# Kernel optimization log

Hardware: AMD Instinct MI355X
Metric: run time of the kernel (lower is better)

## Reference

```python
import jax, jax.numpy as jnp
import numpy as np

B, S, E, H = 2, 2048, 2048, 16
D = E // H  # head_dim = 128


def _rope_tables(seq_len, dim):
    # standard RoPE: theta_i = 10000^(-2i/dim), angles duplicated over pair halves
    inv_freq = 1.0 / (10000.0 ** (np.arange(0, dim, 2, dtype=np.float32) / dim))
    angles = np.arange(seq_len, dtype=np.float32)[:, None] * inv_freq[None, :]  # [S, D/2]
    angles = np.concatenate([angles, angles], axis=-1)  # [S, D]
    return jnp.asarray(np.cos(angles)), jnp.asarray(np.sin(angles))


def setup_inputs() -> dict:
    key = jax.random.key(0)
    ks = jax.random.split(key, 10)
    sc = 1.0 / np.sqrt(E)
    cos, sin = _rope_tables(S, D)
    mask = jnp.tril(jnp.ones((S, S), dtype=bool))[None, None]  # causal [1,1,S,S]
    return {
        "x_q": jax.random.normal(ks[0], (B, S, E), jnp.float32),
        "x_kv": jax.random.normal(ks[1], (B, S, E), jnp.float32),
        "cos": cos,
        "sin": sin,
        "wq": jax.random.normal(ks[2], (E, E), jnp.float32) * sc,
        "bq": jax.random.normal(ks[3], (E,), jnp.float32) * 0.01,
        "wk": jax.random.normal(ks[4], (E, E), jnp.float32) * sc,
        "bk": jax.random.normal(ks[5], (E,), jnp.float32) * 0.01,
        "wv": jax.random.normal(ks[6], (E, E), jnp.float32) * sc,
        "bv": jax.random.normal(ks[7], (E,), jnp.float32) * 0.01,
        "wo": jax.random.normal(ks[8], (E, E), jnp.float32) * sc,
        "bo": jax.random.normal(ks[9], (E,), jnp.float32) * 0.01,
        "mask": mask,
    }


def _apply_rope(x, cos, sin):
    # x: [B,H,S,D]; cos/sin: [S,D]. rotate-half convention.
    x1, x2 = jnp.split(x, 2, axis=-1)
    rot = jnp.concatenate([-x2, x1], axis=-1)
    return x * cos[None, None] + rot * sin[None, None]


def reference(x_q, x_kv, cos, sin, wq, bq, wk, bk, wv, bv, wo, bo, mask):
    b, sq, _ = x_q.shape
    skv = x_kv.shape[1]
    q = (x_q @ wq.T + bq).reshape(b, sq, H, D).transpose(0, 2, 1, 3)   # [B,H,Sq,D]
    k = (x_kv @ wk.T + bk).reshape(b, skv, H, D).transpose(0, 2, 1, 3)
    v = (x_kv @ wv.T + bv).reshape(b, skv, H, D).transpose(0, 2, 1, 3)
    q = _apply_rope(q, cos, sin)
    k = _apply_rope(k, cos, sin)
    scores = jnp.einsum("bhqd,bhkd->bhqk", q, k) / jnp.sqrt(jnp.float32(D))
    scores = jnp.where(mask, scores, jnp.float32(-1e9))
    w = jax.nn.softmax(scores, axis=-1)  # dropout p=0 -> identity
    out = jnp.einsum("bhqk,bhkd->bhqd", w, v)
    out = out.transpose(0, 2, 1, 3).reshape(b, sq, H * D)
    return out @ wo.T + bo
```

## Files before the change

kernel.cpp:

```cpp
#include <hip/hip_runtime.h>
#include <hip/hip_bf16.h>

#define Bb 2
#define Ss 2048
#define Ee 2048
#define Hh 16
#define Dd 128
#define Mrows (Bb*Ss)

typedef short short8 __attribute__((ext_vector_type(8)));
typedef float f32x4 __attribute__((ext_vector_type(4)));

__device__ __forceinline__ unsigned short bf_rne(float f) {
    unsigned u = __builtin_bit_cast(unsigned, f);
    u += 0x7fffu + ((u >> 16) & 1u);
    return (unsigned short)(u >> 16);
}
__device__ __forceinline__ float bf2f(unsigned short x) {
    unsigned u = ((unsigned)x) << 16;
    return __builtin_bit_cast(float, u);
}
__device__ __forceinline__ void load_lds16(const void* g, void* l) {
    __builtin_amdgcn_global_load_lds(
        (const __attribute__((address_space(1))) unsigned int*)g,
        (__attribute__((address_space(3))) unsigned int*)l, 16, 0, 0);
}

__global__ void cast_all_kernel(const float4* __restrict__ xq, const float4* __restrict__ xkv,
                                const float4* __restrict__ wq, const float4* __restrict__ wk,
                                const float4* __restrict__ wv, const float4* __restrict__ wo,
                                ushort4* __restrict__ out) {
    int i = blockIdx.x * 256 + threadIdx.x;
    const float4* src;
    int rel;
    if (i < 2097152)       { src = xq;  rel = i; }
    else if (i < 4194304)  { src = xkv; rel = i - 2097152; }
    else if (i < 5242880)  { src = wq;  rel = i - 4194304; }
    else if (i < 6291456)  { src = wk;  rel = i - 5242880; }
    else if (i < 7340032)  { src = wv;  rel = i - 6291456; }
    else                   { src = wo;  rel = i - 7340032; }
    float4 v = src[rel];
    ushort4 o;
    o.x = bf_rne(v.x); o.y = bf_rne(v.y); o.z = bf_rne(v.z); o.w = bf_rne(v.w);
    out[i] = o;
}

#define NTK 64
#define BUFB 24576

__device__ __forceinline__ void gemm_core(
    const short* __restrict__ A, const short* __restrict__ W,
    int m0, int n0, char* lds, f32x4 (&acc)[8][4], int tid)
{
    const int wid  = tid >> 6, lane = tid & 63;
    const int wr   = wid >> 1, wc   = wid & 1;
    const int quad = lane >> 4, l16 = lane & 15;
    const int lr   = lane >> 3, sl  = lane & 7;
    const int g    = sl ^ lr;
    const int grow = 2*(wid*8 + lr) + (g >> 2);
    const int kcol = (g & 3) * 8;
    const int cx16 = ((((l16 & 1) << 2) + quad) ^ ((l16 >> 1) & 7)) << 4;
    const int arow = (l16 >> 1) << 7;

    const short* Ab = A + (size_t)(m0 + grow) * Ee + kcol;
    const short* Wb = W + (size_t)(n0 + grow) * Ee + kcol;

    auto stageTile = [&](int kt, int so) {
        const short* a = Ab + kt * 32;
        const short* w = Wb + kt * 32;
        #pragma unroll
        for (int i = 0; i < 4; ++i)
            load_lds16(a + (size_t)i*64*Ee, lds + so + i*4096 + wid*1024);
        #pragma unroll
        for (int i = 0; i < 2; ++i)
            load_lds16(w + (size_t)i*64*Ee, lds + so + 16384 + i*4096 + wid*1024);
    };

    stageTile(0, 0);
    stageTile(1, BUFB);
    asm volatile("s_waitcnt vmcnt(6)\n\ts_barrier" ::: "memory");

    int bo = 0, so = 2*BUFB;
    for (int t = 0; t < NTK; ++t) {
        if (t + 2 < NTK) stageTile(t + 2, so);

        const char* Abase = lds + bo + wr*8192 + arow + cx16;
        const char* Bbase = lds + bo + 16384 + wc*4096 + arow + cx16;
        short8 af[8], bf[4];
        #pragma unroll
        for (int i = 0; i < 8; ++i) af[i] = *(const short8*)(Abase + i*1024);
        #pragma unroll
        for (int j = 0; j < 4; ++j) bf[j] = *(const short8*)(Bbase + j*1024);

        __builtin_amdgcn_s_setprio(1);
        #pragma unroll
        for (int i = 0; i < 8; ++i)
            #pragma unroll
            for (int j = 0; j < 4; ++j)
                acc[i][j] = __builtin_amdgcn_mfma_f32_16x16x32_bf16(af[i], bf[j], acc[i][j], 0, 0, 0);
        __builtin_amdgcn_s_setprio(0);

        if (t == NTK - 1) break;
        if (t < NTK - 2) asm volatile("s_waitcnt vmcnt(6)\n\ts_barrier" ::: "memory");
        else             asm volatile("s_waitcnt vmcnt(0)\n\ts_barrier" ::: "memory");
        bo = (bo == 2*BUFB) ? 0 : bo + BUFB;
        so = (so == 2*BUFB) ? 0 : so + BUFB;
    }
}

__global__ __launch_bounds__(256, 2) void qkv_gemm(
    const short* __restrict__ xq, const short* __restrict__ xkv,
    const short* __restrict__ wq, const short* __restrict__ wk, const short* __restrict__ wv,
    const float* __restrict__ bq, const float* __restrict__ bk, const float* __restrict__ bv,
    short* __restrict__ Qr, short* __restrict__ Kr, short* __restrict__ VT)
{
    __shared__ __align__(16) char lds[73728];
    const int tid  = threadIdx.x;
    const int wid  = tid >> 6, lane = tid & 63;
    const int quad = lane >> 4, l16 = lane & 15;
    const int wr   = wid >> 1, wc   = wid & 1;
    const int m0   = blockIdx.x * 256;
    const int sub  = blockIdx.y >> 4;
    const int nb   = blockIdx.y & 15;
    const int n0   = nb * 128;

    const short* A = (sub == 0) ? xq : xkv;
    const short* W = (sub == 0) ? wq : (sub == 1) ? wk : wv;
    const float* bias = (sub == 0) ? bq : (sub == 1) ? bk : bv;

    f32x4 acc[8][4] = {};
    gemm_core(A, W, m0, n0, lds, acc, tid);

    const int b0 = m0 >> 11;
    const int s0 = m0 & (Ss - 1);

    if (sub < 2) {
        short* out = sub ? Kr : Qr;
        #pragma unroll
        for (int i = 0; i < 8; ++i)
            #pragma unroll
            for (int j = 0; j < 4; ++j)
                #pragma unroll
                for (int r = 0; r < 4; ++r) {
                    int gm = m0 + wr*128 + i*16 + quad*4 + r;
                    int d  = wc*64 + j*16 + l16;
                    float v = acc[i][j][r] + bias[n0 + d];
                    int b = gm >> 11, s = gm & (Ss - 1);
                    out[(((size_t)(b*Hh + nb)) * Ss + s) * Dd + d] = (short)bf_rne(v);
                }
    } else {
        __syncthreads();
        short* T = (short*)lds + wid * 8704;
        #pragma unroll
        for (int i = 0; i < 8; ++i)
            #pragma unroll
            for (int j = 0; j < 4; ++j)
                #pragma unroll
                for (int r = 0; r < 4; ++r) {
                    int dl  = j*16 + l16;
                    int slc = i*16 + quad*4 + r;
                    T[dl*136 + slc] = (short)bf_rne(acc[i][j][r] + bias[n0 + wc*64 + dl]);
                }
        __syncthreads();
        #pragma unroll
        for (int ss = 0; ss < 16; ++ss) {
            short8 v = *(const short8*)&T[lane*136 + ss*8];
            int dg = wc*64 + lane;
            int sg = s0 + wr*128 + ss*8;
            *(short8*)&VT[(((size_t)(b0*Hh + nb)) * Dd + dg) * Ss + sg] = v;
        }
    }
}

__global__ __launch_bounds__(256, 2) void oproj_gemm(
    const short* __restrict__ A, const short* __restrict__ W,
    const float* __restrict__ bias, float* __restrict__ Cf)
{
    __shared__ __align__(16) char lds[73728];
    const int tid  = threadIdx.x;
    const int wid  = tid >> 6, lane = tid & 63;
    const int quad = lane >> 4, l16 = lane & 15;
    const int wr   = wid >> 1, wc   = wid & 1;
    const int m0   = blockIdx.x * 256;
    const int n0   = blockIdx.y * 128;

    f32x4 acc[8][4] = {};
    gemm_core(A, W, m0, n0, lds, acc, tid);

    #pragma unroll
    for (int i = 0; i < 8; ++i)
        #pragma unroll
        for (int j = 0; j < 4; ++j)
            #pragma unroll
            for (int r = 0; r < 4; ++r) {
                int gm = m0 + wr*128 + i*16 + quad*4 + r;
                int gn = n0 + wc*64 + j*16 + l16;
                Cf[(size_t)gm * Ee + gn] = acc[i][j][r] + bias[gn];
            }
}

__global__ void rope_kernel(short* __restrict__ Qr, short* __restrict__ Kr,
                            const float* __restrict__ cosT, const float* __restrict__ sinT) {
    short* X    = blockIdx.y ? Kr : Qr;
    float scale = blockIdx.y ? 1.0f : 0.08838834764831845f;
    int idx = blockIdx.x * 256 + threadIdx.x;
    int d  = idx & 63;
    int s  = (idx >> 6) & (Ss - 1);
    int bh = idx >> 17;
    size_t base = ((size_t)bh * Ss + s) * Dd;
    float x1 = bf2f((unsigned short)X[base + d]);
    float x2 = bf2f((unsigned short)X[base + d + 64]);
    float c  = cosT[s*Dd + d];
    float sn = sinT[s*Dd + d];
    X[base + d]      = (short)bf_rne((x1 * c - x2 * sn) * scale);
    X[base + d + 64] = (short)bf_rne((x2 * c + x1 * sn) * scale);
}

__global__ __launch_bounds__(256, 2) void attn_kernel(
    const short* __restrict__ Q, const short* __restrict__ Kk,
    const short* __restrict__ VT, short* __restrict__ O)
{
    __shared__ short Ks[64*128];
    __shared__ short Vt[2][128*64];
    __shared__ short Pw[4][32*72];

    const int tid  = threadIdx.x;
    const int wave = tid >> 6;
    const int lane = tid & 63;
    const int quad = lane >> 4;
    const int l16  = lane & 15;
    const int mmap = (blockIdx.x + blockIdx.y) & 15;
    const int qt   = (blockIdx.y & 16) ? (15 - mmap) : mmap;
    const int bh = blockIdx.y;
    const int b  = bh >> 4, h = bh & 15;
    const size_t head_off = (size_t)bh * Ss * Dd;
    const short* Kg  = Kk + head_off;
    const short* VTg = VT + head_off;

    auto stageK = [&](int kt) {
        #pragma unroll
        for (int j = 0; j < 4; ++j) {
            int r = wave*16 + j*4 + (lane >> 4);
            int c = (lane & 15) ^ (r & 15);
            load_lds16(Kg + (size_t)(kt*64 + r)*Dd + c*8, &Ks[(wave*16 + j*4)*128]);
        }
    };
    auto stageV = [&](int kt, int buf) {
        #pragma unroll
        for (int j = 0; j < 4; ++j) {
            int r = wave*32 + j*8 + (lane >> 3);
            int c = (lane & 7) ^ (r & 7);
            load_lds16(VTg + (size_t)r*Ss + kt*64 + c*8, &Vt[buf][(wave*32 + j*8)*64]);
        }
    };

    const int qbase = qt*128 + wave*32;
    short8 qf[2][4];
    #pragma unroll
    for (int mi = 0; mi < 2; ++mi)
        #pragma unroll
        for (int ds = 0; ds < 4; ++ds)
            qf[mi][ds] = *(const short8*)&Q[head_off + (size_t)(qbase + mi*16 + l16)*Dd + ds*32 + quad*8];

    f32x4 o[2][8] = {};
    float m_i[2][4], l_i[2][4];
    #pragma unroll
    for (int mi = 0; mi < 2; ++mi)
        #pragma unroll
        for (int r = 0; r < 4; ++r) { m_i[mi][r] = -__builtin_inff(); l_i[mi][r] = 0.f; }

    const int ktiles = 2*qt + 2;
    stageK(0);
    stageV(0, 0);

    for (int kt = 0; kt < ktiles; ++kt) {
        __syncthreads();
        if (kt + 1 < ktiles) stageV(kt+1, (kt+1)&1);

        f32x4 sc[2][4] = {};
        #pragma unroll
        for (int jk = 0; jk < 4; ++jk)
            #pragma unroll
            for (int ds = 0; ds < 4; ++ds) {
                short8 kf = *(const short8*)&Ks[(jk*16 + l16)*128 + (((ds*4 + quad) ^ l16) * 8)];
                #pragma unroll
                for (int mi = 0; mi < 2; ++mi)
                    sc[mi][jk] = __builtin_amdgcn_mfma_f32_16x16x32_bf16(qf[mi][ds], kf, sc[mi][jk], 0, 0, 0);
            }

        __syncthreads();
        if (kt + 1 < ktiles) stageK(kt+1);

        const int k0 = kt*64;
        #pragma unroll
        for (int mi = 0; mi < 2; ++mi) {
            if (k0 + 63 > qbase + mi*16) {
                #pragma unroll
                for (int jk = 0; jk < 4; ++jk) {
                    int kg = k0 + jk*16 + l16;
                    #pragma unroll
                    for (int r = 0; r < 4; ++r)
                        if (kg > qbase + mi*16 + quad*4 + r) sc[mi][jk][r] = -__builtin_inff();
                }
            }
        }

        float alpha[2][4];
        #pragma unroll
        for (int mi = 0; mi < 2; ++mi)
            #pragma unroll
            for (int r = 0; r < 4; ++r) {
                float mx = fmaxf(fmaxf(sc[mi][0][r], sc[mi][1][r]), fmaxf(sc[mi][2][r], sc[mi][3][r]));
                #pragma unroll
                for (int off = 1; off < 16; off <<= 1)
                    mx = fmaxf(mx, __shfl_xor(mx, off));
                float mn = fmaxf(m_i[mi][r], mx);
                alpha[mi][r] = __expf(m_i[mi][r] - mn);
                m_i[mi][r] = mn;
                float s = 0.f;
                #pragma unroll
                for (int jk = 0; jk < 4; ++jk) {
                    float p = __expf(sc[mi][jk][r] - mn);
                    sc[mi][jk][r] = p;
                    s += p;
                }
                l_i[mi][r] = l_i[mi][r] * alpha[mi][r] + s;
            }

        #pragma unroll
        for (int mi = 0; mi < 2; ++mi)
            #pragma unroll
            for (int jk = 0; jk < 4; ++jk)
                #pragma unroll
                for (int r = 0; r < 4; ++r)
                    Pw[wave][(mi*16 + quad*4 + r)*72 + jk*16 + l16] = (short)bf_rne(sc[mi][jk][r]);

        #pragma unroll
        for (int mi = 0; mi < 2; ++mi)
            #pragma unroll
            for (int dt = 0; dt < 8; ++dt)
                #pragma unroll
                for (int r = 0; r < 4; ++r)
                    o[mi][dt][r] *= alpha[mi][r];

        short8 pa[2][2];
        #pragma unroll
        for (int mi = 0; mi < 2; ++mi)
            #pragma unroll
            for (int kk = 0; kk < 2; ++kk)
                pa[mi][kk] = *(const short8*)&Pw[wave][(mi*16 + l16)*72 + kk*32 + quad*8];

        const short* vb = Vt[kt & 1];
        #pragma unroll
        for (int dt = 0; dt < 8; ++dt)
            #pragma unroll
            for (int kk = 0; kk < 2; ++kk) {
                short8 vf = *(const short8*)&vb[(dt*16 + l16)*64 + (((kk*4 + quad) ^ (l16 & 7)) * 8)];
                #pragma unroll
                for (int mi = 0; mi < 2; ++mi)
                    o[mi][dt] = __builtin_amdgcn_mfma_f32_16x16x32_bf16(pa[mi][kk], vf, o[mi][dt], 0, 0, 0);
            }
    }

    #pragma unroll
    for (int mi = 0; mi < 2; ++mi)
        #pragma unroll
        for (int r = 0; r < 4; ++r) {
            float l = l_i[mi][r];
            #pragma unroll
            for (int off = 1; off < 16; off <<= 1)
                l += __shfl_xor(l, off);
            float inv = 1.0f / l;
            int srow = qbase + mi*16 + quad*4 + r;
            size_t obase = ((size_t)b * Ss + srow) * Ee + h * Dd;
            #pragma unroll
            for (int dt = 0; dt < 8; ++dt)
                O[obase + dt*16 + l16] = (short)bf_rne(o[mi][dt][r] * inv);
        }
}

extern "C" void kernel_launch(void* const* d_in, const int* in_sizes, int n_in,
                              void* d_out, int out_size, void* d_ws, size_t ws_size,
                              hipStream_t stream) {
    const float* x_q  = (const float*)d_in[0];
    const float* x_kv = (const float*)d_in[1];
    const float* cosT = (const float*)d_in[2];
    const float* sinT = (const float*)d_in[3];
    const float* wq = (const float*)d_in[4];
    const float* bq = (const float*)d_in[5];
    const float* wk = (const float*)d_in[6];
    const float* bk = (const float*)d_in[7];
    const float* wv = (const float*)d_in[8];
    const float* bv = (const float*)d_in[9];
    const float* wo = (const float*)d_in[10];
    const float* bo = (const float*)d_in[11];

    size_t off = 0;
    auto alloc = [&](size_t bytes) {
        void* p = (char*)d_ws + off;
        off += (bytes + 255) & ~(size_t)255;
        return p;
    };
    const size_t nX = (size_t)Mrows * Ee;
    const size_t nW = (size_t)Ee * Ee;
    short* xq16  = (short*)alloc(nX * 2);
    short* xkv16 = (short*)alloc(nX * 2);
    short* wq16  = (short*)alloc(nW * 2);
    short* wk16  = (short*)alloc(nW * 2);
    short* wv16  = (short*)alloc(nW * 2);
    short* wo16  = (short*)alloc(nW * 2);
    short* Qr    = (short*)alloc(nX * 2);
    short* Kr    = (short*)alloc(nX * 2);
    short* VTb   = (short*)alloc(nX * 2);
    short* Ob    = (short*)alloc(nX * 2);

    cast_all_kernel<<<32768, 256, 0, stream>>>(
        (const float4*)x_q, (const float4*)x_kv, (const float4*)wq,
        (const float4*)wk, (const float4*)wv, (const float4*)wo, (ushort4*)xq16);

    qkv_gemm<<<dim3(Mrows/256, 48), 256, 0, stream>>>(
        xq16, xkv16, wq16, wk16, wv16, bq, bk, bv, Qr, Kr, VTb);

    rope_kernel<<<dim3((Bb*Hh*Ss*64)/256, 2), 256, 0, stream>>>(Qr, Kr, cosT, sinT);

    attn_kernel<<<dim3(16, Bb*Hh), 256, 0, stream>>>(Qr, Kr, VTb, Ob);

    oproj_gemm<<<dim3(Mrows/256, Ee/128), 256, 0, stream>>>(Ob, wo16, bo, (float*)d_out);
}
```

Before: 440.6 us.

## Switch QKV GEMM to double-buffered LDS pipeline to fit three blocks per CU

The QKV projection GEMM moves from a triple-buffered LDS ring (72 KB) to a new double-buffered core (48 KB) and raises launch bounds to 3 blocks per CU. A-fragments are now loaded one at a time inside the MFMA loop, which lowers register pressure. The V-transpose epilogue runs in two halves so it fits the smaller LDS buffer. The aim is higher occupancy to hide latency. The cost is a full vmcnt(0) wait plus barrier every K-step, which exposes load latency more than the old prefetch-two-ahead scheme did, and tighter register limits may cause spills.

```diff
diff --git a/kernel.cpp b/kernel.cpp
--- a/kernel.cpp
+++ b/kernel.cpp
@@ -46,6 +46,63 @@
 }
 
 #define NTK 64
+
+__device__ __forceinline__ void gemm_core_db(
+    const short* __restrict__ A, const short* __restrict__ W,
+    int m0, int n0, char* lds, f32x4 (&acc)[8][4], int tid)
+{
+    const int wid  = tid >> 6, lane = tid & 63;
+    const int wr   = wid >> 1, wc   = wid & 1;
+    const int quad = lane >> 4, l16 = lane & 15;
+    const int lr   = lane >> 3, sl  = lane & 7;
+    const int g    = sl ^ lr;
+    const int grow = 2*(wid*8 + lr) + (g >> 2);
+    const int kcol = (g & 3) * 8;
+    const int cx16 = ((((l16 & 1) << 2) + quad) ^ ((l16 >> 1) & 7)) << 4;
+    const int arow = (l16 >> 1) << 7;
+
+    const short* Ap = A + (size_t)(m0 + grow) * Ee + kcol;
+    const short* Wp = W + (size_t)(n0 + grow) * Ee + kcol;
+
+    #pragma unroll
+    for (int i = 0; i < 4; ++i)
+        load_lds16(Ap + (size_t)i*64*Ee, lds + i*4096 + wid*1024);
+    #pragma unroll
+    for (int i = 0; i < 2; ++i)
+        load_lds16(Wp + (size_t)i*64*Ee, lds + 16384 + i*4096 + wid*1024);
+    Ap += 32; Wp += 32;
+    asm volatile("s_waitcnt vmcnt(0)\n\ts_barrier" ::: "memory");
+
+    for (int t = 0; t < NTK; ++t) {
+        const int bo = (t & 1) ? 24576 : 0;
+        if (t + 1 < NTK) {
+            const int so = bo ^ 24576;
+            #pragma unroll
+            for (int i = 0; i < 4; ++i)
+                load_lds16(Ap + (size_t)i*64*Ee, lds + so + i*4096 + wid*1024);
+            #pragma unroll
+            for (int i = 0; i < 2; ++i)
+                load_lds16(Wp + (size_t)i*64*Ee, lds + so + 16384 + i*4096 + wid*1024);
+            Ap += 32; Wp += 32;
+        }
+        const char* Ab2 = lds + bo + wr*8192 + arow + cx16;
+        const char* Bb2 = lds + bo + 16384 + wc*4096 + arow + cx16;
+        short8 bfr[4];
+        #pragma unroll
+        for (int j = 0; j < 4; ++j) bfr[j] = *(const short8*)(Bb2 + j*1024);
+        __builtin_amdgcn_s_setprio(1);
+        #pragma unroll
+        for (int i = 0; i < 8; ++i) {
+            short8 af = *(const short8*)(Ab2 + i*1024);
+            #pragma unroll
+            for (int j = 0; j < 4; ++j)
+                acc[i][j] = __builtin_amdgcn_mfma_f32_16x16x32_bf16(af, bfr[j], acc[i][j], 0, 0, 0);
+        }
+        __builtin_amdgcn_s_setprio(0);
+        asm volatile("s_waitcnt vmcnt(0)\n\ts_barrier" ::: "memory");
+    }
+}
+
 #define BUFB 24576
 
 __device__ __forceinline__ void gemm_core(
@@ -86,18 +143,18 @@
 
         const char* Abase = lds + bo + wr*8192 + arow + cx16;
         const char* Bbase = lds + bo + 16384 + wc*4096 + arow + cx16;
-        short8 af[8], bf[4];
+        short8 af[8], bfr[4];
         #pragma unroll
         for (int i = 0; i < 8; ++i) af[i] = *(const short8*)(Abase + i*1024);
         #pragma unroll
-        for (int j = 0; j < 4; ++j) bf[j] = *(const short8*)(Bbase + j*1024);
+        for (int j = 0; j < 4; ++j) bfr[j] = *(const short8*)(Bbase + j*1024);
 
         __builtin_amdgcn_s_setprio(1);
         #pragma unroll
         for (int i = 0; i < 8; ++i)
             #pragma unroll
             for (int j = 0; j < 4; ++j)
-                acc[i][j] = __builtin_amdgcn_mfma_f32_16x16x32_bf16(af[i], bf[j], acc[i][j], 0, 0, 0);
+                acc[i][j] = __builtin_amdgcn_mfma_f32_16x16x32_bf16(af[i], bfr[j], acc[i][j], 0, 0, 0);
         __builtin_amdgcn_s_setprio(0);
 
         if (t == NTK - 1) break;
@@ -108,13 +165,13 @@
     }
 }
 
-__global__ __launch_bounds__(256, 2) void qkv_gemm(
+__global__ __launch_bounds__(256, 3) void qkv_gemm(
     const short* __restrict__ xq, const short* __restrict__ xkv,
     const short* __restrict__ wq, const short* __restrict__ wk, const short* __restrict__ wv,
     const float* __restrict__ bq, const float* __restrict__ bk, const float* __restrict__ bv,
     short* __restrict__ Qr, short* __restrict__ Kr, short* __restrict__ VT)
 {
-    __shared__ __align__(16) char lds[73728];
+    __shared__ __align__(16) char lds[49152];
     const int tid  = threadIdx.x;
     const int wid  = tid >> 6, lane = tid & 63;
     const int quad = lane >> 4, l16 = lane & 15;
@@ -129,7 +186,7 @@
     const float* bias = (sub == 0) ? bq : (sub == 1) ? bk : bv;
 
     f32x4 acc[8][4] = {};
-    gemm_core(A, W, m0, n0, lds, acc, tid);
+    gemm_core_db(A, W, m0, n0, lds, acc, tid);
 
     const int b0 = m0 >> 11;
     const int s0 = m0 & (Ss - 1);
@@ -150,24 +207,27 @@
                 }
     } else {
         __syncthreads();
-        short* T = (short*)lds + wid * 8704;
-        #pragma unroll
-        for (int i = 0; i < 8; ++i)
-            #pragma unroll
-            for (int j = 0; j < 4; ++j)
-                #pragma unroll
-                for (int r = 0; r < 4; ++r) {
-                    int dl  = j*16 + l16;
-                    int slc = i*16 + quad*4 + r;
-                    T[dl*136 + slc] = (short)bf_rne(acc[i][j][r] + bias[n0 + wc*64 + dl]);
-                }
-        __syncthreads();
-        #pragma unroll
-        for (int ss = 0; ss < 16; ++ss) {
-            short8 v = *(const short8*)&T[lane*136 + ss*8];
-            int dg = wc*64 + lane;
-            int sg = s0 + wr*128 + ss*8;
-            *(short8*)&VT[(((size_t)(b0*Hh + nb)) * Dd + dg) * Ss + sg] = v;
+        short* T = (short*)lds + wid * 4608;
+        #pragma unroll
+        for (int h = 0; h < 2; ++h) {
+            #pragma unroll
+            for (int i2 = 0; i2 < 4; ++i2) {
+                #pragma unroll
+                for (int j = 0; j < 4; ++j)
+                    #pragma unroll
+                    for (int r = 0; r < 4; ++r) {
+                        int dl  = j*16 + l16;
+                        int slc = i2*16 + quad*4 + r;
+                        T[dl*72 + slc] = (short)bf_rne(acc[h*4 + i2][j][r] + bias[n0 + wc*64 + dl]);
+                    }
+            }
+            #pragma unroll
+            for (int ss = 0; ss < 8; ++ss) {
+                short8 v = *(const short8*)&T[lane*72 + ss*8];
+                int dg = wc*64 + lane;
+                int sg = s0 + wr*128 + h*64 + ss*8;
+                *(short8*)&VT[(((size_t)(b0*Hh + nb)) * Dd + dg) * Ss + sg] = v;
+            }
         }
     }
 }
```

Measured after the change: 436.8 us. About the same (-0.9%).

## Restructure projection GEMMs to 8-wave blocks with split-phase K=64 pipeline

Applied to the files above, without the earlier changes.

Replaces the 4-wave GEMM core with an 8-wave (512-thread) version that stages K=64 tiles in three 48KB LDS buffers. Each tile is processed in two phases, with barrier-bracketed MFMA bursts interleaved with the LDS fragment reads and the async global-to-LDS loads. Each wave now owns a 64x64 output tile instead of 128x64, which halves accumulator registers per wave and adds more explicit scheduling fences. The intent is better overlap of memory and matrix-core work for the QKV and output projections. The cost is 144KB of LDS per block, which limits occupancy to one block per CU, plus extra barriers per tile.

```diff
diff --git a/kernel.cpp b/kernel.cpp
--- a/kernel.cpp
+++ b/kernel.cpp
@@ -45,76 +45,102 @@
     out[i] = o;
 }
 
-#define NTK 64
-#define BUFB 24576
-
-__device__ __forceinline__ void gemm_core(
+#define NT8 32
+#define BUF8 49152
+
+__device__ __forceinline__ void gemm_core8(
     const short* __restrict__ A, const short* __restrict__ W,
-    int m0, int n0, char* lds, f32x4 (&acc)[8][4], int tid)
+    int m0, int n0, char* lds, f32x4 (&acc)[4][4], int tid)
 {
     const int wid  = tid >> 6, lane = tid & 63;
     const int wr   = wid >> 1, wc   = wid & 1;
     const int quad = lane >> 4, l16 = lane & 15;
     const int lr   = lane >> 3, sl  = lane & 7;
     const int g    = sl ^ lr;
-    const int grow = 2*(wid*8 + lr) + (g >> 2);
-    const int kcol = (g & 3) * 8;
-    const int cx16 = ((((l16 & 1) << 2) + quad) ^ ((l16 >> 1) & 7)) << 4;
-    const int arow = (l16 >> 1) << 7;
-
-    const short* Ab = A + (size_t)(m0 + grow) * Ee + kcol;
-    const short* Wb = W + (size_t)(n0 + grow) * Ee + kcol;
-
-    auto stageTile = [&](int kt, int so) {
-        const short* a = Ab + kt * 32;
-        const short* w = Wb + kt * 32;
-        #pragma unroll
-        for (int i = 0; i < 4; ++i)
-            load_lds16(a + (size_t)i*64*Ee, lds + so + i*4096 + wid*1024);
-        #pragma unroll
-        for (int i = 0; i < 2; ++i)
-            load_lds16(w + (size_t)i*64*Ee, lds + so + 16384 + i*4096 + wid*1024);
+
+    const short* Ap = A + (size_t)(m0 + wid*8 + lr) * Ee + g*8;
+    const short* Wp = W + (size_t)(n0 + wid*8 + lr) * Ee + g*8;
+
+    auto stageHalf = [&](int kt, int so, int ih) {
+        #pragma unroll
+        for (int i = 0; i < 2; ++i) {
+            int is = ih*2 + i;
+            load_lds16(Ap + (size_t)is*64*Ee + kt*64, lds + so + is*8192 + wid*1024);
+        }
+        load_lds16(Wp + (size_t)ih*64*Ee + kt*64, lds + so + 32768 + ih*8192 + wid*1024);
     };
 
-    stageTile(0, 0);
-    stageTile(1, BUFB);
+    const int arow = (wr*64 + l16) * 128;
+    const int brow = (wc*64 + l16) * 128;
+
+    #define LDSFRAGS(bo, ks)                                                          \
+        {                                                                             \
+            const int cofs = (((ks)*4 + quad) ^ (l16 & 7)) << 4;                      \
+            _Pragma("unroll")                                                         \
+            for (int i2 = 0; i2 < 4; ++i2)                                            \
+                af[i2] = *(const short8*)(lds + (bo) + arow + i2*2048 + cofs);        \
+            _Pragma("unroll")                                                         \
+            for (int j = 0; j < 4; ++j)                                               \
+                bfr[j] = *(const short8*)(lds + (bo) + 32768 + brow + j*2048 + cofs); \
+        }
+
+    #define MFMA16()                                                                  \
+        {                                                                             \
+            __builtin_amdgcn_s_setprio(1);                                            \
+            _Pragma("unroll")                                                         \
+            for (int i2 = 0; i2 < 4; ++i2)                                            \
+                _Pragma("unroll")                                                     \
+                for (int j = 0; j < 4; ++j)                                           \
+                    acc[i2][j] = __builtin_amdgcn_mfma_f32_16x16x32_bf16(             \
+                        af[i2], bfr[j], acc[i2][j], 0, 0, 0);                         \
+            __builtin_amdgcn_s_setprio(0);                                            \
+        }
+
+    #define PHASE_ENTER()                                                             \
+        __builtin_amdgcn_s_barrier();                                                 \
+        asm volatile("s_waitcnt lgkmcnt(0)" ::: "memory");                            \
+        __builtin_amdgcn_sched_barrier(0);
+
+    #define PHASE_EXIT()                                                              \
+        __builtin_amdgcn_sched_barrier(0);                                            \
+        __builtin_amdgcn_s_barrier();
+
+    stageHalf(0, 0, 0);    stageHalf(0, 0, 1);
+    stageHalf(1, BUF8, 0); stageHalf(1, BUF8, 1);
     asm volatile("s_waitcnt vmcnt(6)\n\ts_barrier" ::: "memory");
 
-    int bo = 0, so = 2*BUFB;
-    for (int t = 0; t < NTK; ++t) {
-        if (t + 2 < NTK) stageTile(t + 2, so);
-
-        const char* Abase = lds + bo + wr*8192 + arow + cx16;
-        const char* Bbase = lds + bo + 16384 + wc*4096 + arow + cx16;
-        short8 af[8], bf[4];
-        #pragma unroll
-        for (int i = 0; i < 8; ++i) af[i] = *(const short8*)(Abase + i*1024);
-        #pragma unroll
-        for (int j = 0; j < 4; ++j) bf[j] = *(const short8*)(Bbase + j*1024);
-
-        __builtin_amdgcn_s_setprio(1);
-        #pragma unroll
-        for (int i = 0; i < 8; ++i)
-            #pragma unroll
-            for (int j = 0; j < 4; ++j)
-                acc[i][j] = __builtin_amdgcn_mfma_f32_16x16x32_bf16(af[i], bf[j], acc[i][j], 0, 0, 0);
-        __builtin_amdgcn_s_setprio(0);
-
-        if (t == NTK - 1) break;
-        if (t < NTK - 2) asm volatile("s_waitcnt vmcnt(6)\n\ts_barrier" ::: "memory");
+    int bo = 0, so = 2*BUF8;
+    for (int t = 0; t < NT8; ++t) {
+        short8 af[4], bfr[4];
+        LDSFRAGS(bo, 0)
+        if (t + 2 < NT8) stageHalf(t+2, so, 0);
+        PHASE_ENTER()
+        MFMA16()
+        PHASE_EXIT()
+        LDSFRAGS(bo, 1)
+        if (t + 2 < NT8) stageHalf(t+2, so, 1);
+        PHASE_ENTER()
+        MFMA16()
+        __builtin_amdgcn_sched_barrier(0);
+        if (t == NT8 - 1) break;
+        if (t < NT8 - 2) asm volatile("s_waitcnt vmcnt(6)\n\ts_barrier" ::: "memory");
         else             asm volatile("s_waitcnt vmcnt(0)\n\ts_barrier" ::: "memory");
-        bo = (bo == 2*BUFB) ? 0 : bo + BUFB;
-        so = (so == 2*BUFB) ? 0 : so + BUFB;
+        bo = (bo == 2*BUF8) ? 0 : bo + BUF8;
+        so = (so == 2*BUF8) ? 0 : so + BUF8;
     }
-}
-
-__global__ __launch_bounds__(256, 2) void qkv_gemm(
+    #undef LDSFRAGS
+    #undef MFMA16
+    #undef PHASE_ENTER
+    #undef PHASE_EXIT
+}
+
+__global__ __launch_bounds__(512, 2) void qkv_gemm(
     const short* __restrict__ xq, const short* __restrict__ xkv,
     const short* __restrict__ wq, const short* __restrict__ wk, const short* __restrict__ wv,
     const float* __restrict__ bq, const float* __restrict__ bk, const float* __restrict__ bv,
     short* __restrict__ Qr, short* __restrict__ Kr, short* __restrict__ VT)
 {
-    __shared__ __align__(16) char lds[73728];
+    __shared__ __align__(16) char lds[147456];
     const int tid  = threadIdx.x;
     const int wid  = tid >> 6, lane = tid & 63;
     const int quad = lane >> 4, l16 = lane & 15;
@@ -128,8 +154,8 @@
     const short* W = (sub == 0) ? wq : (sub == 1) ? wk : wv;
     const float* bias = (sub == 0) ? bq : (sub == 1) ? bk : bv;
 
-    f32x4 acc[8][4] = {};
-    gemm_core(A, W, m0, n0, lds, acc, tid);
+    f32x4 acc[4][4] = {};
+    gemm_core8(A, W, m0, n0, lds, acc, tid);
 
     const int b0 = m0 >> 11;
     const int s0 = m0 & (Ss - 1);
@@ -137,46 +163,46 @@
     if (sub < 2) {
         short* out = sub ? Kr : Qr;
         #pragma unroll
-        for (int i = 0; i < 8; ++i)
+        for (int i2 = 0; i2 < 4; ++i2)
             #pragma unroll
             for (int j = 0; j < 4; ++j)
                 #pragma unroll
                 for (int r = 0; r < 4; ++r) {
-                    int gm = m0 + wr*128 + i*16 + quad*4 + r;
+                    int gm = m0 + wr*64 + i2*16 + quad*4 + r;
                     int d  = wc*64 + j*16 + l16;
-                    float v = acc[i][j][r] + bias[n0 + d];
+                    float v = acc[i2][j][r] + bias[n0 + d];
                     int b = gm >> 11, s = gm & (Ss - 1);
                     out[(((size_t)(b*Hh + nb)) * Ss + s) * Dd + d] = (short)bf_rne(v);
                 }
     } else {
         __syncthreads();
-        short* T = (short*)lds + wid * 8704;
-        #pragma unroll
-        for (int i = 0; i < 8; ++i)
+        short* T = (short*)lds + wid * 4608;
+        #pragma unroll
+        for (int i2 = 0; i2 < 4; ++i2)
             #pragma unroll
             for (int j = 0; j < 4; ++j)
                 #pragma unroll
                 for (int r = 0; r < 4; ++r) {
                     int dl  = j*16 + l16;
-                    int slc = i*16 + quad*4 + r;
-                    T[dl*136 + slc] = (short)bf_rne(acc[i][j][r] + bias[n0 + wc*64 + dl]);
+                    int slc = i2*16 + quad*4 + r;
+                    T[dl*72 + slc] = (short)bf_rne(acc[i2][j][r] + bias[n0 + wc*64 + dl]);
                 }
         __syncthreads();
         #pragma unroll
-        for (int ss = 0; ss < 16; ++ss) {
-            short8 v = *(const short8*)&T[lane*136 + ss*8];
+        for (int ss = 0; ss < 8; ++ss) {
+            short8 v = *(const short8*)&T[lane*72 + ss*8];
             int dg = wc*64 + lane;
-            int sg = s0 + wr*128 + ss*8;
+            int sg = s0 + wr*64 + ss*8;
             *(short8*)&VT[(((size_t)(b0*Hh + nb)) * Dd + dg) * Ss + sg] = v;
         }
     }
 }
 
-__global__ __launch_bounds__(256, 2) void oproj_gemm(
+__global__ __launch_bounds__(512, 2) void oproj_gemm(
     const short* __restrict__ A, const short* __restrict__ W,
     const float* __restrict__ bias, float* __restrict__ Cf)
 {
-    __shared__ __align__(16) char lds[73728];
+    __shared__ __align__(16) char lds[147456];
     const int tid  = threadIdx.x;
     const int wid  = tid >> 6, lane = tid & 63;
     const int quad = lane >> 4, l16 = lane & 15;
@@ -184,18 +210,18 @@
     const int m0   = blockIdx.x * 256;
     const int n0   = blockIdx.y * 128;
 
-    f32x4 acc[8][4] = {};
-    gemm_core(A, W, m0, n0, lds, acc, tid);
+    f32x4 acc[4][4] = {};
+    gemm_core8(A, W, m0, n0, lds, acc, tid);
 
     #pragma unroll
-    for (int i = 0; i < 8; ++i)
+    for (int i2 = 0; i2 < 4; ++i2)
         #pragma unroll
         for (int j = 0; j < 4; ++j)
             #pragma unroll
             for (int r = 0; r < 4; ++r) {
-                int gm = m0 + wr*128 + i*16 + quad*4 + r;
+                int gm = m0 + wr*64 + i2*16 + quad*4 + r;
                 int gn = n0 + wc*64 + j*16 + l16;
-                Cf[(size_t)gm * Ee + gn] = acc[i][j][r] + bias[gn];
+                Cf[(size_t)gm * Ee + gn] = acc[i2][j][r] + bias[gn];
             }
 }
 
@@ -418,12 +444,12 @@
         (const float4*)x_q, (const float4*)x_kv, (const float4*)wq,
         (const float4*)wk, (const float4*)wv, (const float4*)wo, (ushort4*)xq16);
 
-    qkv_gemm<<<dim3(Mrows/256, 48), 256, 0, stream>>>(
+    qkv_gemm<<<dim3(Mrows/256, 48), 512, 0, stream>>>(
         xq16, xkv16, wq16, wk16, wv16, bq, bk, bv, Qr, Kr, VTb);
 
     rope_kernel<<<dim3((Bb*Hh*Ss*64)/256, 2), 256, 0, stream>>>(Qr, Kr, cosT, sinT);
 
     attn_kernel<<<dim3(16, Bb*Hh), 256, 0, stream>>>(Qr, Kr, VTb, Ob);
 
-    oproj_gemm<<<dim3(Mrows/256, Ee/128), 256, 0, stream>>>(Ob, wo16, bo, (float*)d_out);
-}
+    oproj_gemm<<<dim3(Mrows/256, Ee/128), 512, 0, stream>>>(Ob, wo16, bo, (float*)d_out);
+}
```

Result: no change. 441.7 us (+0.2%).
